# Optimization experiments

Measured on AMD Instinct MI355X. Metric: run time of the kernel, lower is better.

Reference implementation:

```python
import jax, jax.numpy as jnp
import numpy as np

SM_SCALE = 1.0 / np.sqrt(64.0)  # 1/sqrt(dim_qk)


def setup_inputs() -> dict:
    key = jax.random.key(0)
    k1, k2, k3 = jax.random.split(key, 3)
    B, S, H, Hkv, Dqk, Dv = 1, 4096, 8, 2, 64, 64
    q = jax.random.normal(k1, (B, S, H, Dqk), dtype=jnp.float32)
    k = jax.random.normal(k2, (B, S, Hkv, Dqk), dtype=jnp.float32)
    v = jax.random.normal(k3, (B, S, Hkv, Dv), dtype=jnp.float32)
    return {"q": q, "k": k, "v": v}


def reference(q, k, v):
    # q: [B,S,H,Dqk], k: [B,S,Hkv,Dqk], v: [B,S,Hkv,Dv]; query head h uses kv head h // groups
    B, S, H, Dqk = q.shape
    Hkv = k.shape[2]
    G = H // Hkv  # groups per kv head
    k_exp = jnp.repeat(k, G, axis=2)  # [B,S,H,Dqk], head h -> kv head h//G
    v_exp = jnp.repeat(v, G, axis=2)  # [B,S,H,Dv]
    scores = jnp.einsum('bqhd,bkhd->bhqk', q, k_exp) * SM_SCALE  # [B,H,S,S]
    # causal mask: query i attends to keys j <= i
    qi = jnp.arange(S)[:, None]
    kj = jnp.arange(S)[None, :]
    scores = jnp.where(qi >= kj, scores, -jnp.inf)
    p = jax.nn.softmax(scores, axis=-1)  # online-softmax result, computed densely
    out = jnp.einsum('bhqk,bkhd->bqhd', p, v_exp)  # [B,S,H,Dv]
    return out
```

## Files before the change

### kernel.cpp

```cpp
#include <hip/hip_runtime.h>
#include <hip/hip_bf16.h>

typedef __attribute__((ext_vector_type(8))) __bf16 bf16x8;
typedef __attribute__((ext_vector_type(4))) __bf16 bf16x4;
typedef __attribute__((ext_vector_type(2))) __bf16 bf16x2;
typedef __attribute__((ext_vector_type(4))) float f32x4;
typedef __attribute__((ext_vector_type(16))) float f32x16;
typedef __attribute__((ext_vector_type(2))) int i32x2;

constexpr int S_LEN = 4096;
constexpr int H = 8;
constexpr int HKV = 2;
constexpr int D = 64;
constexpr int BK = 64;
constexpr int QW = 32;
constexpr int WAVES = 4;
constexpr int QB_ROWS = QW * WAVES;
constexpr int NQB = S_LEN / QB_ROWS;
constexpr int NKT = S_LEN / BK;
constexpr float QSCALE = 0.125f * 1.44269504088896f;

__device__ __forceinline__ float fexp2(float x) {
  return __builtin_amdgcn_exp2f(x);
}

__device__ __forceinline__ int swz(int row, int col) {
  return (row * 64 + col) ^ ((((row >> 2) ^ row) & 7) << 3);
}

#define GLOAD_LDS16(g, l)                                        \
  __builtin_amdgcn_global_load_lds(                              \
      (const __attribute__((address_space(1))) void*)(g),        \
      (__attribute__((address_space(3))) void*)(l), 16, 0, 0)

__device__ __forceinline__ bf16x8 load8_scaled(const float* p, float scale) {
  f32x4 a = *reinterpret_cast<const f32x4*>(p);
  f32x4 b = *reinterpret_cast<const f32x4*>(p + 4);
  bf16x8 r;
  r[0] = (__bf16)(a[0] * scale); r[1] = (__bf16)(a[1] * scale);
  r[2] = (__bf16)(a[2] * scale); r[3] = (__bf16)(a[3] * scale);
  r[4] = (__bf16)(b[0] * scale); r[5] = (__bf16)(b[1] * scale);
  r[6] = (__bf16)(b[2] * scale); r[7] = (__bf16)(b[3] * scale);
  return r;
}

__device__ __forceinline__ int pk2(float lo, float hi) {
  bf16x2 t;
  t[0] = (__bf16)lo;
  t[1] = (__bf16)hi;
  return __builtin_bit_cast(int, t);
}

__global__ __launch_bounds__(256) void pack_kv_kernel(
    const float* __restrict__ k, const float* __restrict__ v,
    __bf16* __restrict__ kp, __bf16* __restrict__ vp) {
  const int tid  = threadIdx.x;
  const int tile = blockIdx.x & (NKT - 1);
  const int hkv  = blockIdx.x >> 6;
  const int kv0  = tile * BK;
  __bf16* kb = kp + (size_t)(hkv * NKT + tile) * 4096;
  __bf16* vb = vp + (size_t)(hkv * NKT + tile) * 4096;
  {
    const int row = tid >> 2, cg = (tid & 3) * 16;
    const float* src = k + ((size_t)(kv0 + row) * HKV + hkv) * D + cg;
    bf16x8 w0, w1;
#pragma unroll
    for (int j = 0; j < 8; ++j) w0[j] = (__bf16)src[j];
#pragma unroll
    for (int j = 0; j < 8; ++j) w1[j] = (__bf16)src[8 + j];
    *reinterpret_cast<bf16x8*>(&kb[swz(row, cg)]) = w0;
    *reinterpret_cast<bf16x8*>(&kb[swz(row, cg + 8)]) = w1;
  }
  {
    const int s16 = tid >> 4, s4 = (tid & 15) * 4;
    f32x4 lv[4];
#pragma unroll
    for (int u = 0; u < 4; ++u)
      lv[u] = *reinterpret_cast<const f32x4*>(
          v + ((size_t)(kv0 + s16 * 4 + u) * HKV + hkv) * D + s4);
#pragma unroll
    for (int j = 0; j < 4; ++j) {
      bf16x4 vw;
      vw[0] = (__bf16)lv[0][j]; vw[1] = (__bf16)lv[1][j];
      vw[2] = (__bf16)lv[2][j]; vw[3] = (__bf16)lv[3][j];
      *reinterpret_cast<bf16x4*>(&vb[swz(s4 + j, s16 * 4)]) = vw;
    }
  }
}

template <int LOG2C, bool SPLIT, bool PACKED>
__global__ __launch_bounds__(256, 3) void gqa_fwd_kernel(
    const float* __restrict__ q, const float* __restrict__ k,
    const float* __restrict__ v, float* __restrict__ out,
    const __bf16* __restrict__ kp, const __bf16* __restrict__ vp,
    __bf16* __restrict__ po, float* __restrict__ ml) {
  constexpr int TPC = (1 << LOG2C) / BK;

  const int tid  = threadIdx.x;
  const int lane = tid & 63;
  const int wid  = tid >> 6;
  const int cl   = lane & 31;
  const int hi   = lane >> 5;

  const int h = blockIdx.x & 7;
  const int widx = blockIdx.x >> 3;
  int qb = 0, c = 0;
  {
    int acc0 = 0;
    for (int qq = NQB - 1; qq >= 0; --qq) {
      const int n = ((qq * QB_ROWS + QB_ROWS - 1) >> LOG2C) + 1;
      if (widx < acc0 + n) { qb = qq; c = widx - acc0; break; }
      acc0 += n;
    }
  }
  const int cmax = (qb * QB_ROWS + QB_ROWS - 1) >> LOG2C;
  const int hkv = h >> 2;
  const int q0w = qb * QB_ROWS + wid * QW;
  const int nt  = (c < cmax) ? TPC : ((QB_ROWS / BK) * (qb + 1) - TPC * cmax);
  const int kb0 = c << LOG2C;
  const int qq  = q0w + cl;

  __shared__ __bf16 klds[2][64 * 64];
  __shared__ __bf16 vlds[2][64 * 64];

  bf16x8 qf[4];
#pragma unroll
  for (int s = 0; s < 4; ++s)
    qf[s] = load8_scaled(q + ((size_t)qq * H + h) * D + s * 16 + hi * 8, QSCALE);

  float l_ = 0.0f;
  f32x16 oa[2];
#pragma unroll
  for (int dt = 0; dt < 2; ++dt)
#pragma unroll
    for (int e = 0; e < 16; ++e) oa[dt][e] = 0.f;

  const int s16 = tid >> 4;
  const int s4  = (tid & 15) * 4;
  auto stage = [&](int buf, int t) {
    if constexpr (PACKED) {
      const size_t blob = (size_t)(hkv * NKT + (kb0 >> 6) + t) * 4096;
      const char* kg = (const char*)(kp + blob) + wid * 2048 + (lane << 4);
      const char* vg = (const char*)(vp + blob) + wid * 2048 + (lane << 4);
      char* kl = (char*)&klds[buf][0] + wid * 2048;
      char* vl = (char*)&vlds[buf][0] + wid * 2048;
      GLOAD_LDS16(kg, kl);
      GLOAD_LDS16(kg + 1024, kl + 1024);
      GLOAD_LDS16(vg, vl);
      GLOAD_LDS16(vg + 1024, vl + 1024);
    } else {
      const int kb = kb0 + t * BK;
#pragma unroll
      for (int u = 0; u < 4; ++u) {
        f32x4 ka = *reinterpret_cast<const f32x4*>(
            k + ((size_t)(kb + u * 16 + s16) * HKV + hkv) * D + s4);
        bf16x4 kw;
        kw[0] = (__bf16)ka[0]; kw[1] = (__bf16)ka[1];
        kw[2] = (__bf16)ka[2]; kw[3] = (__bf16)ka[3];
        *reinterpret_cast<bf16x4*>(&klds[buf][swz(u * 16 + s16, s4)]) = kw;
      }
      f32x4 lv[4];
#pragma unroll
      for (int u = 0; u < 4; ++u)
        lv[u] = *reinterpret_cast<const f32x4*>(
            v + ((size_t)(kb + s16 * 4 + u) * HKV + hkv) * D + s4);
#pragma unroll
      for (int j = 0; j < 4; ++j) {
        bf16x4 vw;
        vw[0] = (__bf16)lv[0][j]; vw[1] = (__bf16)lv[1][j];
        vw[2] = (__bf16)lv[2][j]; vw[3] = (__bf16)lv[3][j];
        *reinterpret_cast<bf16x4*>(&vlds[buf][swz(s4 + j, s16 * 4)]) = vw;
      }
    }
  };

  auto tile_body = [&](int buf, int t) {
    const int kb = kb0 + t * BK;
    if (kb > q0w + 31) return;

    f32x16 st[2];
#pragma unroll
    for (int kt = 0; kt < 2; ++kt)
#pragma unroll
      for (int e = 0; e < 16; ++e) st[kt][e] = 0.f;
    __builtin_amdgcn_s_setprio(1);
#pragma unroll
    for (int s = 0; s < 4; ++s) {
      bf16x8 kf0 = *reinterpret_cast<const bf16x8*>(
          &klds[buf][swz(cl, s * 16 + hi * 8)]);
      bf16x8 kf1 = *reinterpret_cast<const bf16x8*>(
          &klds[buf][swz(32 + cl, s * 16 + hi * 8)]);
      st[0] = __builtin_amdgcn_mfma_f32_32x32x16_bf16(kf0, qf[s], st[0], 0, 0, 0);
      st[1] = __builtin_amdgcn_mfma_f32_32x32x16_bf16(kf1, qf[s], st[1], 0, 0, 0);
    }
    __builtin_amdgcn_s_setprio(0);

    if (kb + 63 > q0w) {
#pragma unroll
      for (int kt = 0; kt < 2; ++kt)
#pragma unroll
        for (int rr = 0; rr < 16; ++rr) {
          const int key = kb + 32 * kt + (rr & 3) + 8 * (rr >> 2) + 4 * hi;
          if (key > qq) st[kt][rr] = -1e30f;
        }
    }

    float ps0 = 0.f, ps1 = 0.f;
#pragma unroll
    for (int kt = 0; kt < 2; ++kt)
#pragma unroll
      for (int e = 0; e < 8; ++e) {
        const float pa = fexp2(st[kt][e]);
        const float pb = fexp2(st[kt][8 + e]);
        ps0 += pa; ps1 += pb;
        st[kt][e] = pa; st[kt][8 + e] = pb;
      }
    l_ += ps0 + ps1;

    __builtin_amdgcn_s_setprio(1);
#pragma unroll
    for (int s = 0; s < 4; ++s) {
      const int kt = s >> 1;
      const int g  = (s & 1) * 2;
      const int x0 = pk2(st[kt][4 * g + 0], st[kt][4 * g + 1]);
      const int x1 = pk2(st[kt][4 * g + 2], st[kt][4 * g + 3]);
      const int y0 = pk2(st[kt][4 * g + 4], st[kt][4 * g + 5]);
      const int y1 = pk2(st[kt][4 * g + 6], st[kt][4 * g + 7]);
      i32x2 w0 = __builtin_amdgcn_permlane32_swap(x0, y0, false, false);
      i32x2 w1 = __builtin_amdgcn_permlane32_swap(x1, y1, false, false);
      int pu[4];
      pu[0] = w0[0]; pu[1] = w1[0]; pu[2] = w0[1]; pu[3] = w1[1];
      bf16x8 pf;
      memcpy(&pf, pu, 16);
      bf16x8 vf0 = *reinterpret_cast<const bf16x8*>(
          &vlds[buf][swz(cl, s * 16 + hi * 8)]);
      bf16x8 vf1 = *reinterpret_cast<const bf16x8*>(
          &vlds[buf][swz(32 + cl, s * 16 + hi * 8)]);
      oa[0] = __builtin_amdgcn_mfma_f32_32x32x16_bf16(vf0, pf, oa[0], 0, 0, 0);
      oa[1] = __builtin_amdgcn_mfma_f32_32x32x16_bf16(vf1, pf, oa[1], 0, 0, 0);
    }
    __builtin_amdgcn_s_setprio(0);
  };

  stage(0, 0);
  __syncthreads();

  for (int t = 0; t < nt; t += 2) {
    if (t + 1 < nt) stage(1, t + 1);
    tile_body(0, t);
    __syncthreads();
    if (t + 2 < nt) stage(0, t + 2);
    tile_body(1, t + 1);
    __syncthreads();
  }

  float lsum = l_ + __shfl_xor(l_, 32, 64);
  if (SPLIT && cmax > 0) {
    __bf16* prow = po + ((size_t)(c * S_LEN + qq) * H + h) * D;
#pragma unroll
    for (int dt = 0; dt < 2; ++dt)
#pragma unroll
      for (int qd = 0; qd < 4; ++qd) {
        bf16x4 pb;
        pb[0] = (__bf16)oa[dt][4 * qd + 0]; pb[1] = (__bf16)oa[dt][4 * qd + 1];
        pb[2] = (__bf16)oa[dt][4 * qd + 2]; pb[3] = (__bf16)oa[dt][4 * qd + 3];
        *reinterpret_cast<bf16x4*>(prow + dt * 32 + qd * 8 + hi * 4) = pb;
      }
    if (lane < 32) ml[(size_t)(c * S_LEN + qq) * H + h] = lsum;
  } else {
    const float inv = 1.0f / lsum;
    float* orow = out + ((size_t)qq * H + h) * D;
#pragma unroll
    for (int dt = 0; dt < 2; ++dt)
#pragma unroll
      for (int qd = 0; qd < 4; ++qd) {
        f32x4 o;
        o[0] = oa[dt][4 * qd + 0] * inv; o[1] = oa[dt][4 * qd + 1] * inv;
        o[2] = oa[dt][4 * qd + 2] * inv; o[3] = oa[dt][4 * qd + 3] * inv;
        *reinterpret_cast<f32x4*>(orow + dt * 32 + qd * 8 + hi * 4) = o;
      }
  }
}

template <int LOG2C>
__global__ __launch_bounds__(256) void combine_kernel(
    const __bf16* __restrict__ po, const float* __restrict__ ml,
    float* __restrict__ out) {
  const int tid = threadIdx.x;
  const int rl  = tid >> 3;
  const int d0  = (tid & 7) * 8;
  const int h   = blockIdx.x & 7;
  const int row = (1 << LOG2C) + (blockIdx.x >> 3) * 32 + rl;
  const int cmax = row >> LOG2C;

  float lsum = 0.f;
  float osum[8];
#pragma unroll
  for (int j = 0; j < 8; ++j) osum[j] = 0.f;
  for (int cc = 0; cc <= cmax; ++cc) {
    const size_t base = (size_t)(cc * S_LEN + row) * H + h;
    lsum += ml[base];
    bf16x8 pv = *reinterpret_cast<const bf16x8*>(po + base * D + d0);
#pragma unroll
    for (int j = 0; j < 8; ++j) osum[j] += (float)pv[j];
  }
  const float inv = 1.0f / lsum;
  float* orow = out + ((size_t)row * H + h) * D + d0;
  f32x4 o0, o1;
  o0[0] = osum[0] * inv; o0[1] = osum[1] * inv;
  o0[2] = osum[2] * inv; o0[3] = osum[3] * inv;
  o1[0] = osum[4] * inv; o1[1] = osum[5] * inv;
  o1[2] = osum[6] * inv; o1[3] = osum[7] * inv;
  *reinterpret_cast<f32x4*>(orow) = o0;
  *reinterpret_cast<f32x4*>(orow + 4) = o1;
}

static int nwork_items(int log2c) {
  int s = 0;
  for (int qb = 0; qb < NQB; ++qb)
    s += ((qb * QB_ROWS + QB_ROWS - 1) >> log2c) + 1;
  return s;
}

extern "C" void kernel_launch(void* const* d_in, const int* in_sizes, int n_in,
                              void* d_out, int out_size, void* d_ws, size_t ws_size,
                              hipStream_t stream) {
  const float* q = (const float*)d_in[0];
  const float* k = (const float*)d_in[1];
  const float* v = (const float*)d_in[2];
  float* out = (float*)d_out;

  const size_t pack_e = (size_t)S_LEN * HKV * D;
  const size_t po8 = 8ull * S_LEN * H * D, ml8 = 8ull * S_LEN * H;
  const size_t po4 = 4ull * S_LEN * H * D, ml4 = 4ull * S_LEN * H;
  const size_t pack_b = pack_e * 2 * sizeof(__bf16);

  __bf16* kp = (__bf16*)d_ws;
  __bf16* vp = kp + pack_e;
  char* rest = (char*)d_ws + pack_b;

  if (ws_size >= pack_b + po8 * 2 + ml8 * 4) {
    __bf16* po = (__bf16*)rest;
    float* mlp = (float*)(rest + po8 * 2);
    pack_kv_kernel<<<dim3(HKV * NKT), dim3(256), 0, stream>>>(k, v, kp, vp);
    gqa_fwd_kernel<9, true, true><<<dim3(8 * nwork_items(9)), dim3(256), 0, stream>>>(
        q, k, v, out, kp, vp, po, mlp);
    combine_kernel<9><<<dim3((S_LEN - 512) / 32 * 8), dim3(256), 0, stream>>>(po, mlp, out);
  } else if (ws_size >= pack_b + po4 * 2 + ml4 * 4) {
    __bf16* po = (__bf16*)rest;
    float* mlp = (float*)(rest + po4 * 2);
    pack_kv_kernel<<<dim3(HKV * NKT), dim3(256), 0, stream>>>(k, v, kp, vp);
    gqa_fwd_kernel<10, true, true><<<dim3(8 * nwork_items(10)), dim3(256), 0, stream>>>(
        q, k, v, out, kp, vp, po, mlp);
    combine_kernel<10><<<dim3((S_LEN - 1024) / 32 * 8), dim3(256), 0, stream>>>(po, mlp, out);
  } else if (ws_size >= pack_b) {
    pack_kv_kernel<<<dim3(HKV * NKT), dim3(256), 0, stream>>>(k, v, kp, vp);
    gqa_fwd_kernel<12, false, true><<<dim3(8 * nwork_items(12)), dim3(256), 0, stream>>>(
        q, k, v, out, kp, vp, nullptr, nullptr);
  } else {
    gqa_fwd_kernel<12, false, false><<<dim3(8 * nwork_items(12)), dim3(256), 0, stream>>>(
        q, k, v, out, nullptr, nullptr, nullptr, nullptr);
  }
}
```

Baseline: 45.96 us.

## Process two query heads per block sharing each staged K/V tile

Each block now computes two query heads that map to the same KV head. Each K/V tile staged into LDS and each fragment loaded from it feeds twice as many MFMAs. The grid is halved and per-thread accumulator and score registers double, so launch bounds drop to 2 blocks per CU. This cuts staging and LDS read traffic per unit of work, at the cost of fewer blocks for load balancing and higher register pressure.

Result: slower. 52.34 us (+13.9%).

```diff
diff --git a/kernel.cpp b/kernel.cpp
--- a/kernel.cpp
+++ b/kernel.cpp
@@ -89,7 +89,7 @@
 }
 
 template <int LOG2C, bool SPLIT, bool PACKED>
-__global__ __launch_bounds__(256, 3) void gqa_fwd_kernel(
+__global__ __launch_bounds__(256, 2) void gqa_fwd_kernel(
     const float* __restrict__ q, const float* __restrict__ k,
     const float* __restrict__ v, float* __restrict__ out,
     const __bf16* __restrict__ kp, const __bf16* __restrict__ vp,
@@ -102,19 +102,20 @@
   const int cl   = lane & 31;
   const int hi   = lane >> 5;
 
-  const int h = blockIdx.x & 7;
-  const int widx = blockIdx.x >> 3;
+  const int hp   = blockIdx.x & 3;
+  const int h0   = hp * 2;
+  const int widx = blockIdx.x >> 2;
   int qb = 0, c = 0;
   {
     int acc0 = 0;
-    for (int qq = NQB - 1; qq >= 0; --qq) {
-      const int n = ((qq * QB_ROWS + QB_ROWS - 1) >> LOG2C) + 1;
-      if (widx < acc0 + n) { qb = qq; c = widx - acc0; break; }
+    for (int qx = NQB - 1; qx >= 0; --qx) {
+      const int n = ((qx * QB_ROWS + QB_ROWS - 1) >> LOG2C) + 1;
+      if (widx < acc0 + n) { qb = qx; c = widx - acc0; break; }
       acc0 += n;
     }
   }
   const int cmax = (qb * QB_ROWS + QB_ROWS - 1) >> LOG2C;
-  const int hkv = h >> 2;
+  const int hkv = hp >> 1;
   const int q0w = qb * QB_ROWS + wid * QW;
   const int nt  = (c < cmax) ? TPC : ((QB_ROWS / BK) * (qb + 1) - TPC * cmax);
   const int kb0 = c << LOG2C;
@@ -123,17 +124,22 @@
   __shared__ __bf16 klds[2][64 * 64];
   __shared__ __bf16 vlds[2][64 * 64];
 
-  bf16x8 qf[4];
-#pragma unroll
-  for (int s = 0; s < 4; ++s)
-    qf[s] = load8_scaled(q + ((size_t)qq * H + h) * D + s * 16 + hi * 8, QSCALE);
-
-  float l_ = 0.0f;
-  f32x16 oa[2];
-#pragma unroll
-  for (int dt = 0; dt < 2; ++dt)
-#pragma unroll
-    for (int e = 0; e < 16; ++e) oa[dt][e] = 0.f;
+  bf16x8 qf[2][4];
+#pragma unroll
+  for (int hd = 0; hd < 2; ++hd)
+#pragma unroll
+    for (int s = 0; s < 4; ++s)
+      qf[hd][s] = load8_scaled(
+          q + ((size_t)qq * H + h0 + hd) * D + s * 16 + hi * 8, QSCALE);
+
+  float l_[2] = {0.f, 0.f};
+  f32x16 oa[2][2];
+#pragma unroll
+  for (int hd = 0; hd < 2; ++hd)
+#pragma unroll
+    for (int dt = 0; dt < 2; ++dt)
+#pragma unroll
+      for (int e = 0; e < 16; ++e) oa[hd][dt][e] = 0.f;
 
   const int s16 = tid >> 4;
   const int s4  = (tid & 15) * 4;
@@ -178,11 +184,13 @@
     const int kb = kb0 + t * BK;
     if (kb > q0w + 31) return;
 
-    f32x16 st[2];
-#pragma unroll
-    for (int kt = 0; kt < 2; ++kt)
-#pragma unroll
-      for (int e = 0; e < 16; ++e) st[kt][e] = 0.f;
+    f32x16 st[2][2];
+#pragma unroll
+    for (int hd = 0; hd < 2; ++hd)
+#pragma unroll
+      for (int kt = 0; kt < 2; ++kt)
+#pragma unroll
+        for (int e = 0; e < 16; ++e) st[hd][kt][e] = 0.f;
     __builtin_amdgcn_s_setprio(1);
 #pragma unroll
     for (int s = 0; s < 4; ++s) {
@@ -190,8 +198,10 @@
           &klds[buf][swz(cl, s * 16 + hi * 8)]);
       bf16x8 kf1 = *reinterpret_cast<const bf16x8*>(
           &klds[buf][swz(32 + cl, s * 16 + hi * 8)]);
-      st[0] = __builtin_amdgcn_mfma_f32_32x32x16_bf16(kf0, qf[s], st[0], 0, 0, 0);
-      st[1] = __builtin_amdgcn_mfma_f32_32x32x16_bf16(kf1, qf[s], st[1], 0, 0, 0);
+      st[0][0] = __builtin_amdgcn_mfma_f32_32x32x16_bf16(kf0, qf[0][s], st[0][0], 0, 0, 0);
+      st[0][1] = __builtin_amdgcn_mfma_f32_32x32x16_bf16(kf1, qf[0][s], st[0][1], 0, 0, 0);
+      st[1][0] = __builtin_amdgcn_mfma_f32_32x32x16_bf16(kf0, qf[1][s], st[1][0], 0, 0, 0);
+      st[1][1] = __builtin_amdgcn_mfma_f32_32x32x16_bf16(kf1, qf[1][s], st[1][1], 0, 0, 0);
     }
     __builtin_amdgcn_s_setprio(0);
 
@@ -201,43 +211,49 @@
 #pragma unroll
         for (int rr = 0; rr < 16; ++rr) {
           const int key = kb + 32 * kt + (rr & 3) + 8 * (rr >> 2) + 4 * hi;
-          if (key > qq) st[kt][rr] = -1e30f;
+          if (key > qq) { st[0][kt][rr] = -1e30f; st[1][kt][rr] = -1e30f; }
         }
     }
 
-    float ps0 = 0.f, ps1 = 0.f;
-#pragma unroll
-    for (int kt = 0; kt < 2; ++kt)
-#pragma unroll
-      for (int e = 0; e < 8; ++e) {
-        const float pa = fexp2(st[kt][e]);
-        const float pb = fexp2(st[kt][8 + e]);
-        ps0 += pa; ps1 += pb;
-        st[kt][e] = pa; st[kt][8 + e] = pb;
-      }
-    l_ += ps0 + ps1;
+#pragma unroll
+    for (int hd = 0; hd < 2; ++hd) {
+      float ps0 = 0.f, ps1 = 0.f;
+#pragma unroll
+      for (int kt = 0; kt < 2; ++kt)
+#pragma unroll
+        for (int e = 0; e < 8; ++e) {
+          const float pa = fexp2(st[hd][kt][e]);
+          const float pb = fexp2(st[hd][kt][8 + e]);
+          ps0 += pa; ps1 += pb;
+          st[hd][kt][e] = pa; st[hd][kt][8 + e] = pb;
+        }
+      l_[hd] += ps0 + ps1;
+    }
 
     __builtin_amdgcn_s_setprio(1);
 #pragma unroll
     for (int s = 0; s < 4; ++s) {
       const int kt = s >> 1;
       const int g  = (s & 1) * 2;
-      const int x0 = pk2(st[kt][4 * g + 0], st[kt][4 * g + 1]);
-      const int x1 = pk2(st[kt][4 * g + 2], st[kt][4 * g + 3]);
-      const int y0 = pk2(st[kt][4 * g + 4], st[kt][4 * g + 5]);
-      const int y1 = pk2(st[kt][4 * g + 6], st[kt][4 * g + 7]);
-      i32x2 w0 = __builtin_amdgcn_permlane32_swap(x0, y0, false, false);
-      i32x2 w1 = __builtin_amdgcn_permlane32_swap(x1, y1, false, false);
-      int pu[4];
-      pu[0] = w0[0]; pu[1] = w1[0]; pu[2] = w0[1]; pu[3] = w1[1];
-      bf16x8 pf;
-      memcpy(&pf, pu, 16);
       bf16x8 vf0 = *reinterpret_cast<const bf16x8*>(
           &vlds[buf][swz(cl, s * 16 + hi * 8)]);
       bf16x8 vf1 = *reinterpret_cast<const bf16x8*>(
           &vlds[buf][swz(32 + cl, s * 16 + hi * 8)]);
-      oa[0] = __builtin_amdgcn_mfma_f32_32x32x16_bf16(vf0, pf, oa[0], 0, 0, 0);
-      oa[1] = __builtin_amdgcn_mfma_f32_32x32x16_bf16(vf1, pf, oa[1], 0, 0, 0);
+#pragma unroll
+      for (int hd = 0; hd < 2; ++hd) {
+        const int x0 = pk2(st[hd][kt][4 * g + 0], st[hd][kt][4 * g + 1]);
+        const int x1 = pk2(st[hd][kt][4 * g + 2], st[hd][kt][4 * g + 3]);
+        const int y0 = pk2(st[hd][kt][4 * g + 4], st[hd][kt][4 * g + 5]);
+        const int y1 = pk2(st[hd][kt][4 * g + 6], st[hd][kt][4 * g + 7]);
+        i32x2 w0 = __builtin_amdgcn_permlane32_swap(x0, y0, false, false);
+        i32x2 w1 = __builtin_amdgcn_permlane32_swap(x1, y1, false, false);
+        int pu[4];
+        pu[0] = w0[0]; pu[1] = w1[0]; pu[2] = w0[1]; pu[3] = w1[1];
+        bf16x8 pf;
+        memcpy(&pf, pu, 16);
+        oa[hd][0] = __builtin_amdgcn_mfma_f32_32x32x16_bf16(vf0, pf, oa[hd][0], 0, 0, 0);
+        oa[hd][1] = __builtin_amdgcn_mfma_f32_32x32x16_bf16(vf1, pf, oa[hd][1], 0, 0, 0);
+      }
     }
     __builtin_amdgcn_s_setprio(0);
   };
@@ -254,31 +270,35 @@
     __syncthreads();
   }
 
-  float lsum = l_ + __shfl_xor(l_, 32, 64);
-  if (SPLIT && cmax > 0) {
-    __bf16* prow = po + ((size_t)(c * S_LEN + qq) * H + h) * D;
-#pragma unroll
-    for (int dt = 0; dt < 2; ++dt)
-#pragma unroll
-      for (int qd = 0; qd < 4; ++qd) {
-        bf16x4 pb;
-        pb[0] = (__bf16)oa[dt][4 * qd + 0]; pb[1] = (__bf16)oa[dt][4 * qd + 1];
-        pb[2] = (__bf16)oa[dt][4 * qd + 2]; pb[3] = (__bf16)oa[dt][4 * qd + 3];
-        *reinterpret_cast<bf16x4*>(prow + dt * 32 + qd * 8 + hi * 4) = pb;
-      }
-    if (lane < 32) ml[(size_t)(c * S_LEN + qq) * H + h] = lsum;
-  } else {
-    const float inv = 1.0f / lsum;
-    float* orow = out + ((size_t)qq * H + h) * D;
-#pragma unroll
-    for (int dt = 0; dt < 2; ++dt)
-#pragma unroll
-      for (int qd = 0; qd < 4; ++qd) {
-        f32x4 o;
-        o[0] = oa[dt][4 * qd + 0] * inv; o[1] = oa[dt][4 * qd + 1] * inv;
-        o[2] = oa[dt][4 * qd + 2] * inv; o[3] = oa[dt][4 * qd + 3] * inv;
-        *reinterpret_cast<f32x4*>(orow + dt * 32 + qd * 8 + hi * 4) = o;
-      }
+#pragma unroll
+  for (int hd = 0; hd < 2; ++hd) {
+    const float lsum = l_[hd] + __shfl_xor(l_[hd], 32, 64);
+    const int h = h0 + hd;
+    if (SPLIT && cmax > 0) {
+      __bf16* prow = po + ((size_t)(c * S_LEN + qq) * H + h) * D;
+#pragma unroll
+      for (int dt = 0; dt < 2; ++dt)
+#pragma unroll
+        for (int qd = 0; qd < 4; ++qd) {
+          bf16x4 pb;
+          pb[0] = (__bf16)oa[hd][dt][4 * qd + 0]; pb[1] = (__bf16)oa[hd][dt][4 * qd + 1];
+          pb[2] = (__bf16)oa[hd][dt][4 * qd + 2]; pb[3] = (__bf16)oa[hd][dt][4 * qd + 3];
+          *reinterpret_cast<bf16x4*>(prow + dt * 32 + qd * 8 + hi * 4) = pb;
+        }
+      if (lane < 32) ml[(size_t)(c * S_LEN + qq) * H + h] = lsum;
+    } else {
+      const float inv = 1.0f / lsum;
+      float* orow = out + ((size_t)qq * H + h) * D;
+#pragma unroll
+      for (int dt = 0; dt < 2; ++dt)
+#pragma unroll
+        for (int qd = 0; qd < 4; ++qd) {
+          f32x4 o;
+          o[0] = oa[hd][dt][4 * qd + 0] * inv; o[1] = oa[hd][dt][4 * qd + 1] * inv;
+          o[2] = oa[hd][dt][4 * qd + 2] * inv; o[3] = oa[hd][dt][4 * qd + 3] * inv;
+          *reinterpret_cast<f32x4*>(orow + dt * 32 + qd * 8 + hi * 4) = o;
+        }
+    }
   }
 }
 
@@ -343,22 +363,22 @@
     __bf16* po = (__bf16*)rest;
     float* mlp = (float*)(rest + po8 * 2);
     pack_kv_kernel<<<dim3(HKV * NKT), dim3(256), 0, stream>>>(k, v, kp, vp);
-    gqa_fwd_kernel<9, true, true><<<dim3(8 * nwork_items(9)), dim3(256), 0, stream>>>(
+    gqa_fwd_kernel<9, true, true><<<dim3(4 * nwork_items(9)), dim3(256), 0, stream>>>(
         q, k, v, out, kp, vp, po, mlp);
     combine_kernel<9><<<dim3((S_LEN - 512) / 32 * 8), dim3(256), 0, stream>>>(po, mlp, out);
   } else if (ws_size >= pack_b + po4 * 2 + ml4 * 4) {
     __bf16* po = (__bf16*)rest;
     float* mlp = (float*)(rest + po4 * 2);
     pack_kv_kernel<<<dim3(HKV * NKT), dim3(256), 0, stream>>>(k, v, kp, vp);
-    gqa_fwd_kernel<10, true, true><<<dim3(8 * nwork_items(10)), dim3(256), 0, stream>>>(
+    gqa_fwd_kernel<10, true, true><<<dim3(4 * nwork_items(10)), dim3(256), 0, stream>>>(
         q, k, v, out, kp, vp, po, mlp);
     combine_kernel<10><<<dim3((S_LEN - 1024) / 32 * 8), dim3(256), 0, stream>>>(po, mlp, out);
   } else if (ws_size >= pack_b) {
     pack_kv_kernel<<<dim3(HKV * NKT), dim3(256), 0, stream>>>(k, v, kp, vp);
-    gqa_fwd_kernel<12, false, true><<<dim3(8 * nwork_items(12)), dim3(256), 0, stream>>>(
+    gqa_fwd_kernel<12, false, true><<<dim3(4 * nwork_items(12)), dim3(256), 0, stream>>>(
         q, k, v, out, kp, vp, nullptr, nullptr);
   } else {
-    gqa_fwd_kernel<12, false, false><<<dim3(8 * nwork_items(12)), dim3(256), 0, stream>>>(
+    gqa_fwd_kernel<12, false, false><<<dim3(4 * nwork_items(12)), dim3(256), 0, stream>>>(
         q, k, v, out, nullptr, nullptr, nullptr, nullptr);
   }
 }
```

## Load V fragments directly from global memory instead of staging through LDS

Applied to the files above, without the earlier changes.

The packed V tile now uses a plain unswizzled transposed layout so each lane can read its MFMA B-operand fragments straight from global memory (L2) at the start of each tile, and the V LDS double buffer is removed. This halves LDS footprint and LDS traffic per tile, which may raise occupancy and cut LDS bandwidth pressure. The pack kernel is also split into twice as many blocks with vectorized K loads. The cost is global-memory latency on V reads inside the compute loop, which is no longer hidden by the async LDS prefetch, and the unpacked fallback path does very slow scalar gathers.

After: 69.89 us. 52.1% more time.

```diff
diff --git a/kernel.cpp b/kernel.cpp
--- a/kernel.cpp
+++ b/kernel.cpp
@@ -55,35 +55,33 @@
     const float* __restrict__ k, const float* __restrict__ v,
     __bf16* __restrict__ kp, __bf16* __restrict__ vp) {
   const int tid  = threadIdx.x;
-  const int tile = blockIdx.x & (NKT - 1);
-  const int hkv  = blockIdx.x >> 6;
+  const int sb   = blockIdx.x & 1;
+  const int tile = (blockIdx.x >> 1) & (NKT - 1);
+  const int hkv  = blockIdx.x >> 7;
   const int kv0  = tile * BK;
   __bf16* kb = kp + (size_t)(hkv * NKT + tile) * 4096;
   __bf16* vb = vp + (size_t)(hkv * NKT + tile) * 4096;
   {
-    const int row = tid >> 2, cg = (tid & 3) * 16;
+    const int row = sb * 32 + (tid >> 3), cg = (tid & 7) * 8;
     const float* src = k + ((size_t)(kv0 + row) * HKV + hkv) * D + cg;
-    bf16x8 w0, w1;
-#pragma unroll
-    for (int j = 0; j < 8; ++j) w0[j] = (__bf16)src[j];
-#pragma unroll
-    for (int j = 0; j < 8; ++j) w1[j] = (__bf16)src[8 + j];
-    *reinterpret_cast<bf16x8*>(&kb[swz(row, cg)]) = w0;
-    *reinterpret_cast<bf16x8*>(&kb[swz(row, cg + 8)]) = w1;
+    f32x4 a = *reinterpret_cast<const f32x4*>(src);
+    f32x4 b = *reinterpret_cast<const f32x4*>(src + 4);
+    bf16x8 w;
+    w[0] = (__bf16)a[0]; w[1] = (__bf16)a[1]; w[2] = (__bf16)a[2]; w[3] = (__bf16)a[3];
+    w[4] = (__bf16)b[0]; w[5] = (__bf16)b[1]; w[6] = (__bf16)b[2]; w[7] = (__bf16)b[3];
+    *reinterpret_cast<bf16x8*>(&kb[swz(row, cg)]) = w;
   }
   {
-    const int s16 = tid >> 4, s4 = (tid & 15) * 4;
-    f32x4 lv[4];
-#pragma unroll
-    for (int u = 0; u < 4; ++u)
-      lv[u] = *reinterpret_cast<const f32x4*>(
-          v + ((size_t)(kv0 + s16 * 4 + u) * HKV + hkv) * D + s4);
+    const int kvl = sb * 32 + (tid >> 4) * 2, d0 = (tid & 15) * 4;
+    f32x4 lv0 = *reinterpret_cast<const f32x4*>(
+        v + ((size_t)(kv0 + kvl) * HKV + hkv) * D + d0);
+    f32x4 lv1 = *reinterpret_cast<const f32x4*>(
+        v + ((size_t)(kv0 + kvl + 1) * HKV + hkv) * D + d0);
 #pragma unroll
     for (int j = 0; j < 4; ++j) {
-      bf16x4 vw;
-      vw[0] = (__bf16)lv[0][j]; vw[1] = (__bf16)lv[1][j];
-      vw[2] = (__bf16)lv[2][j]; vw[3] = (__bf16)lv[3][j];
-      *reinterpret_cast<bf16x4*>(&vb[swz(s4 + j, s16 * 4)]) = vw;
+      bf16x2 vw;
+      vw[0] = (__bf16)lv0[j]; vw[1] = (__bf16)lv1[j];
+      *reinterpret_cast<bf16x2*>(&vb[(d0 + j) * 64 + kvl]) = vw;
     }
   }
 }
@@ -107,9 +105,9 @@
   int qb = 0, c = 0;
   {
     int acc0 = 0;
-    for (int qq = NQB - 1; qq >= 0; --qq) {
-      const int n = ((qq * QB_ROWS + QB_ROWS - 1) >> LOG2C) + 1;
-      if (widx < acc0 + n) { qb = qq; c = widx - acc0; break; }
+    for (int qx = NQB - 1; qx >= 0; --qx) {
+      const int n = ((qx * QB_ROWS + QB_ROWS - 1) >> LOG2C) + 1;
+      if (widx < acc0 + n) { qb = qx; c = widx - acc0; break; }
       acc0 += n;
     }
   }
@@ -121,7 +119,6 @@
   const int qq  = q0w + cl;
 
   __shared__ __bf16 klds[2][64 * 64];
-  __shared__ __bf16 vlds[2][64 * 64];
 
   bf16x8 qf[4];
 #pragma unroll
@@ -135,20 +132,16 @@
 #pragma unroll
     for (int e = 0; e < 16; ++e) oa[dt][e] = 0.f;
 
-  const int s16 = tid >> 4;
-  const int s4  = (tid & 15) * 4;
   auto stage = [&](int buf, int t) {
     if constexpr (PACKED) {
       const size_t blob = (size_t)(hkv * NKT + (kb0 >> 6) + t) * 4096;
       const char* kg = (const char*)(kp + blob) + wid * 2048 + (lane << 4);
-      const char* vg = (const char*)(vp + blob) + wid * 2048 + (lane << 4);
       char* kl = (char*)&klds[buf][0] + wid * 2048;
-      char* vl = (char*)&vlds[buf][0] + wid * 2048;
       GLOAD_LDS16(kg, kl);
       GLOAD_LDS16(kg + 1024, kl + 1024);
-      GLOAD_LDS16(vg, vl);
-      GLOAD_LDS16(vg + 1024, vl + 1024);
     } else {
+      const int s16 = tid >> 4;
+      const int s4  = (tid & 15) * 4;
       const int kb = kb0 + t * BK;
 #pragma unroll
       for (int u = 0; u < 4; ++u) {
@@ -159,24 +152,34 @@
         kw[2] = (__bf16)ka[2]; kw[3] = (__bf16)ka[3];
         *reinterpret_cast<bf16x4*>(&klds[buf][swz(u * 16 + s16, s4)]) = kw;
       }
-      f32x4 lv[4];
-#pragma unroll
-      for (int u = 0; u < 4; ++u)
-        lv[u] = *reinterpret_cast<const f32x4*>(
-            v + ((size_t)(kb + s16 * 4 + u) * HKV + hkv) * D + s4);
-#pragma unroll
-      for (int j = 0; j < 4; ++j) {
-        bf16x4 vw;
-        vw[0] = (__bf16)lv[0][j]; vw[1] = (__bf16)lv[1][j];
-        vw[2] = (__bf16)lv[2][j]; vw[3] = (__bf16)lv[3][j];
-        *reinterpret_cast<bf16x4*>(&vlds[buf][swz(s4 + j, s16 * 4)]) = vw;
-      }
     }
   };
 
   auto tile_body = [&](int buf, int t) {
     const int kb = kb0 + t * BK;
     if (kb > q0w + 31) return;
+
+    bf16x8 vf[2][4];
+    if constexpr (PACKED) {
+      const __bf16* vt = vp + (size_t)(hkv * NKT + (kb0 >> 6) + t) * 4096;
+#pragma unroll
+      for (int s = 0; s < 4; ++s) {
+        vf[0][s] = *reinterpret_cast<const bf16x8*>(vt + cl * 64 + s * 16 + hi * 8);
+        vf[1][s] = *reinterpret_cast<const bf16x8*>(vt + (32 + cl) * 64 + s * 16 + hi * 8);
+      }
+    } else {
+#pragma unroll
+      for (int s = 0; s < 4; ++s)
+#pragma unroll
+        for (int dt = 0; dt < 2; ++dt) {
+          bf16x8 w;
+#pragma unroll
+          for (int i = 0; i < 8; ++i)
+            w[i] = (__bf16)v[((size_t)(kb + s * 16 + hi * 8 + i) * HKV + hkv) * D +
+                             dt * 32 + cl];
+          vf[dt][s] = w;
+        }
+    }
 
     f32x16 st[2];
 #pragma unroll
@@ -232,12 +235,8 @@
       pu[0] = w0[0]; pu[1] = w1[0]; pu[2] = w0[1]; pu[3] = w1[1];
       bf16x8 pf;
       memcpy(&pf, pu, 16);
-      bf16x8 vf0 = *reinterpret_cast<const bf16x8*>(
-          &vlds[buf][swz(cl, s * 16 + hi * 8)]);
-      bf16x8 vf1 = *reinterpret_cast<const bf16x8*>(
-          &vlds[buf][swz(32 + cl, s * 16 + hi * 8)]);
-      oa[0] = __builtin_amdgcn_mfma_f32_32x32x16_bf16(vf0, pf, oa[0], 0, 0, 0);
-      oa[1] = __builtin_amdgcn_mfma_f32_32x32x16_bf16(vf1, pf, oa[1], 0, 0, 0);
+      oa[0] = __builtin_amdgcn_mfma_f32_32x32x16_bf16(vf[0][s], pf, oa[0], 0, 0, 0);
+      oa[1] = __builtin_amdgcn_mfma_f32_32x32x16_bf16(vf[1][s], pf, oa[1], 0, 0, 0);
     }
     __builtin_amdgcn_s_setprio(0);
   };
@@ -331,30 +330,31 @@
   float* out = (float*)d_out;
 
   const size_t pack_e = (size_t)S_LEN * HKV * D;
-  const size_t po8 = 8ull * S_LEN * H * D, ml8 = 8ull * S_LEN * H;
-  const size_t po4 = 4ull * S_LEN * H * D, ml4 = 4ull * S_LEN * H;
   const size_t pack_b = pack_e * 2 * sizeof(__bf16);
+  auto po_e = [](int ns) { return (size_t)ns * S_LEN * H * D; };
+  auto ml_e = [](int ns) { return (size_t)ns * S_LEN * H; };
 
   __bf16* kp = (__bf16*)d_ws;
   __bf16* vp = kp + pack_e;
   char* rest = (char*)d_ws + pack_b;
-
-  if (ws_size >= pack_b + po8 * 2 + ml8 * 4) {
+  const int npack = 2 * HKV * NKT;
+
+  if (ws_size >= pack_b + po_e(8) * 2 + ml_e(8) * 4) {
     __bf16* po = (__bf16*)rest;
-    float* mlp = (float*)(rest + po8 * 2);
-    pack_kv_kernel<<<dim3(HKV * NKT), dim3(256), 0, stream>>>(k, v, kp, vp);
+    float* mlp = (float*)(rest + po_e(8) * 2);
+    pack_kv_kernel<<<dim3(npack), dim3(256), 0, stream>>>(k, v, kp, vp);
     gqa_fwd_kernel<9, true, true><<<dim3(8 * nwork_items(9)), dim3(256), 0, stream>>>(
         q, k, v, out, kp, vp, po, mlp);
     combine_kernel<9><<<dim3((S_LEN - 512) / 32 * 8), dim3(256), 0, stream>>>(po, mlp, out);
-  } else if (ws_size >= pack_b + po4 * 2 + ml4 * 4) {
+  } else if (ws_size >= pack_b + po_e(4) * 2 + ml_e(4) * 4) {
     __bf16* po = (__bf16*)rest;
-    float* mlp = (float*)(rest + po4 * 2);
-    pack_kv_kernel<<<dim3(HKV * NKT), dim3(256), 0, stream>>>(k, v, kp, vp);
+    float* mlp = (float*)(rest + po_e(4) * 2);
+    pack_kv_kernel<<<dim3(npack), dim3(256), 0, stream>>>(k, v, kp, vp);
     gqa_fwd_kernel<10, true, true><<<dim3(8 * nwork_items(10)), dim3(256), 0, stream>>>(
         q, k, v, out, kp, vp, po, mlp);
     combine_kernel<10><<<dim3((S_LEN - 1024) / 32 * 8), dim3(256), 0, stream>>>(po, mlp, out);
   } else if (ws_size >= pack_b) {
-    pack_kv_kernel<<<dim3(HKV * NKT), dim3(256), 0, stream>>>(k, v, kp, vp);
+    pack_kv_kernel<<<dim3(npack), dim3(256), 0, stream>>>(k, v, kp, vp);
     gqa_fwd_kernel<12, false, true><<<dim3(8 * nwork_items(12)), dim3(256), 0, stream>>>(
         q, k, v, out, kp, vp, nullptr, nullptr);
   } else {
```
